# Kernel optimization log

Measured on AMD Instinct MI355X. Metric: run time of the kernel, lower is better.

Reference implementation:

```python
import jax, jax.numpy as jnp
import numpy as np

N, E = 50000, 800000
IN, HID, HEADS = 512, 64, 2
NEG_SLOPE = 0.2

def _p(key, shape, fan_in):
    return jax.random.normal(key, shape, dtype=jnp.float32) * (1.0 / np.sqrt(fan_in))

def setup_inputs() -> dict:
    key = jax.random.key(0)
    ks = jax.random.split(key, 16)
    x = jax.random.normal(ks[0], (N, IN), dtype=jnp.float32)
    edge_index = jax.random.randint(ks[1], (2, E), 0, N)
    d = dict(x=x, edge_index=edge_index)
    # layer 0: in -> hidden*heads
    d['W0'] = _p(ks[2], (IN, HEADS * HID), IN)
    d['a_src0'] = _p(ks[3], (HEADS, HID), HID)
    d['a_dst0'] = _p(ks[4], (HEADS, HID), HID)
    d['b0'] = jnp.zeros((HEADS * HID,), jnp.float32)
    # layer 1: hidden*heads -> hidden*heads
    d['W1'] = _p(ks[5], (HEADS * HID, HEADS * HID), HEADS * HID)
    d['a_src1'] = _p(ks[6], (HEADS, HID), HID)
    d['a_dst1'] = _p(ks[7], (HEADS, HID), HID)
    d['b1'] = jnp.zeros((HEADS * HID,), jnp.float32)
    # layer 2: hidden*heads -> hidden, heads=1
    d['W2'] = _p(ks[8], (HEADS * HID, HID), HEADS * HID)
    d['a_src2'] = _p(ks[9], (1, HID), HID)
    d['a_dst2'] = _p(ks[10], (1, HID), HID)
    d['b2'] = jnp.zeros((HID,), jnp.float32)
    # MLP heads
    d['Wv'] = _p(ks[11], (HID, HID), HID)
    d['bv'] = jnp.zeros((HID,), jnp.float32)
    d['Wt'] = _p(ks[12], (HID, HID), HID)
    d['bt'] = jnp.zeros((HID,), jnp.float32)
    return d

def gat_conv(x, src, dst, W, a_src, a_dst, b, n_nodes):
    # PyG GATConv: linear -> per-node att scores -> edge leaky_relu -> segment softmax over dst -> weighted scatter-sum
    H, C = a_src.shape
    h = (x @ W).reshape(n_nodes, H, C)                     # [N,H,C]
    s = jnp.einsum('nhc,hc->nh', h, a_src)                 # [N,H]
    t = jnp.einsum('nhc,hc->nh', h, a_dst)                 # [N,H]
    e = jax.nn.leaky_relu(s[src] + t[dst], NEG_SLOPE)      # [Etot,H]
    m = jax.ops.segment_max(e, dst, num_segments=n_nodes)  # stable softmax per dst
    ex = jnp.exp(e - m[dst])
    den = jax.ops.segment_sum(ex, dst, num_segments=n_nodes)
    alpha = ex / (den[dst] + 1e-16)                        # [Etot,H]
    out = jax.ops.segment_sum(h[src] * alpha[..., None], dst, num_segments=n_nodes)
    return out.reshape(n_nodes, H * C) + b

def reference(x, edge_index, W0, a_src0, a_dst0, b0, W1, a_src1, a_dst1, b1,
              W2, a_src2, a_dst2, b2, Wv, bv, Wt, bt):
    n = x.shape[0]
    loop = jnp.arange(n)
    src = jnp.concatenate([edge_index[0], loop])  # add_self_loops=True
    dst = jnp.concatenate([edge_index[1], loop])
    h = gat_conv(x, src, dst, W0, a_src0, a_dst0, b0, n)
    h = jax.nn.relu(h)
    h = gat_conv(h, src, dst, W1, a_src1, a_dst1, b1, n)
    h = jax.nn.relu(h)
    h = gat_conv(h, src, dst, W2, a_src2, a_dst2, b2, n)  # heads=1 -> [N,HID]
    x_vision = jax.nn.relu(h @ Wv + bv)
    x_text = jax.nn.relu(h @ Wt + bt)
    return (h, x_vision, x_text)
```

## Files before the change

kernel.cpp:

```cpp
#include <hip/hip_runtime.h>
#include <hip/hip_bf16.h>
#include <hip/hip_fp16.h>
#include <math.h>

#define NN 50000
#define NE 800000

typedef unsigned short ushort_t;
typedef unsigned int uint_t;
typedef __attribute__((ext_vector_type(8))) short bf16x8;
typedef __attribute__((ext_vector_type(4))) float f32x4;

__device__ __forceinline__ float lrelu(float x) { return x >= 0.f ? x : 0.2f * x; }

__device__ __forceinline__ ushort_t f2bf_rn(float f) {
  uint_t u = __builtin_bit_cast(uint_t, f);
  uint_t r = u + 0x7FFFu + ((u >> 16) & 1u);
  return (ushort_t)(r >> 16);
}
__device__ __forceinline__ float bf2f(ushort_t h) {
  uint_t u = ((uint_t)h) << 16;
  return __builtin_bit_cast(float, u);
}
__device__ __forceinline__ ushort_t f2h_bits(float f) {
  __half h = __float2half(f);
  return __builtin_bit_cast(ushort_t, h);
}

__global__ __launch_bounds__(256) void zero_kernel(int* __restrict__ p, int n) {
  int i = blockIdx.x * 256 + threadIdx.x;
  if (i < n) p[i] = 0;
}

__device__ __forceinline__ void prep_dev(const float* __restrict__ W, int Kdim, int C,
                                         ushort_t* __restrict__ wth, ushort_t* __restrict__ wtl,
                                         int t) {
  int nk = Kdim >> 4;
  if (t >= C * nk) return;
  int c = t / nk, kc = (t % nk) << 4;
  uint_t hw[8], lw[8];
#pragma unroll
  for (int i = 0; i < 8; ++i) {
    float f0 = W[(size_t)(kc + 2 * i) * C + c];
    float f1 = W[(size_t)(kc + 2 * i + 1) * C + c];
    ushort_t h0 = f2bf_rn(f0), h1 = f2bf_rn(f1);
    ushort_t l0 = f2bf_rn(f0 - bf2f(h0)), l1 = f2bf_rn(f1 - bf2f(h1));
    hw[i] = (uint_t)h0 | ((uint_t)h1 << 16);
    lw[i] = (uint_t)l0 | ((uint_t)l1 << 16);
  }
  uint_t* ph = (uint_t*)&wth[(size_t)c * Kdim + kc];
  uint_t* pl = (uint_t*)&wtl[(size_t)c * Kdim + kc];
  *(uint4*)ph = make_uint4(hw[0], hw[1], hw[2], hw[3]);
  *(uint4*)(ph + 4) = make_uint4(hw[4], hw[5], hw[6], hw[7]);
  *(uint4*)pl = make_uint4(lw[0], lw[1], lw[2], lw[3]);
  *(uint4*)(pl + 4) = make_uint4(lw[4], lw[5], lw[6], lw[7]);
}

#define CNT_BLOCKS 3125
__global__ __launch_bounds__(256) void setup_kernel(const int* __restrict__ ei,
                                                    int* __restrict__ counts,
                                                    const float* __restrict__ W0, ushort_t* wt0h, ushort_t* wt0l,
                                                    const float* __restrict__ W1, ushort_t* wt1h, ushort_t* wt1l,
                                                    const float* __restrict__ W2, ushort_t* wt2h, ushort_t* wt2l,
                                                    const float* __restrict__ Wv, const float* __restrict__ Wt,
                                                    ushort_t* wHh, ushort_t* wHl) {
  int b = blockIdx.x;
  if (b < CNT_BLOCKS) {
    int e = b * 256 + threadIdx.x;
    if (e < NE) atomicAdd(&counts[ei[NE + e]], 1);
    return;
  }
  b -= CNT_BLOCKS;
  if (b < 16) { prep_dev(W0, 512, 128, wt0h, wt0l, b * 256 + threadIdx.x); return; }
  b -= 16;
  if (b < 4) { prep_dev(W1, 128, 128, wt1h, wt1l, b * 256 + threadIdx.x); return; }
  b -= 4;
  if (b < 2) { prep_dev(W2, 128, 64, wt2h, wt2l, b * 256 + threadIdx.x); return; }
  b -= 2;
  if (b < 1) { prep_dev(Wv, 64, 64, wHh, wHl, b * 256 + threadIdx.x); return; }
  b -= 1;
  prep_dev(Wt, 64, 64, wHh + 64 * 64, wHl + 64 * 64, b * 256 + threadIdx.x);
}

__global__ __launch_bounds__(256) void scan_blocksum_kernel(const int* __restrict__ counts,
                                                            int* __restrict__ bsums, int n) {
  __shared__ int red[4];
  int i = blockIdx.x * 256 + threadIdx.x;
  int v = (i < n) ? counts[i] : 0;
#pragma unroll
  for (int off = 32; off > 0; off >>= 1) v += __shfl_down(v, off);
  if ((threadIdx.x & 63) == 0) red[threadIdx.x >> 6] = v;
  __syncthreads();
  if (threadIdx.x == 0) bsums[blockIdx.x] = red[0] + red[1] + red[2] + red[3];
}

__global__ __launch_bounds__(256) void scan_offsets_kernel(int* __restrict__ bsums, int nb) {
  __shared__ int sm[256];
  int tid = threadIdx.x;
  int v = (tid < nb) ? bsums[tid] : 0;
  sm[tid] = v;
  __syncthreads();
  for (int off = 1; off < 256; off <<= 1) {
    int u = (tid >= off) ? sm[tid - off] : 0;
    __syncthreads();
    sm[tid] += u;
    __syncthreads();
  }
  if (tid < nb) bsums[tid] = sm[tid] - v;
}

__global__ __launch_bounds__(256) void scan_final_kernel(const int* __restrict__ counts,
                                                         const int* __restrict__ boffs,
                                                         int* __restrict__ row_ptr,
                                                         int* __restrict__ cursor, int n, int E) {
  __shared__ int sm[256];
  int tid = threadIdx.x;
  int i = blockIdx.x * 256 + tid;
  int v = (i < n) ? counts[i] : 0;
  int orig = v;
  sm[tid] = v;
  __syncthreads();
  for (int off = 1; off < 256; off <<= 1) {
    int u = (tid >= off) ? sm[tid - off] : 0;
    __syncthreads();
    sm[tid] += u;
    __syncthreads();
  }
  if (i < n) {
    row_ptr[i] = boffs[blockIdx.x] + sm[tid] - orig;
    cursor[i] = 0;
  }
  if (i == n) row_ptr[n] = E;
}

__global__ void fill_kernel(const int* __restrict__ ei, const int* __restrict__ row_ptr,
                            int* __restrict__ cursor, int* __restrict__ col_src, int E) {
  int e = blockIdx.x * blockDim.x + threadIdx.x;
  if (e < E) {
    int d = ei[E + e];
    int pos = row_ptr[d] + atomicAdd(&cursor[d], 1);
    col_src[pos] = ei[e];
  }
}

template <int K, bool SPLIT>
__global__ __launch_bounds__(256, 4) void gemm_att128_kernel(const float* __restrict__ Af,
                                                             const ushort_t* __restrict__ Ahp,
                                                             const ushort_t* __restrict__ Alp,
                                                             const ushort_t* __restrict__ wth,
                                                             const ushort_t* __restrict__ wtl,
                                                             const float* __restrict__ a_src,
                                                             const float* __restrict__ a_dst,
                                                             __half2* __restrict__ h2h,
                                                             float* __restrict__ s_arr,
                                                             float* __restrict__ t_arr, int n) {
  __shared__ __align__(16) ushort_t smem[15360];
  ushort_t (*ah)[40] = (ushort_t(*)[40])smem;
  ushort_t (*al)[40] = (ushort_t(*)[40])(smem + 2560);
  ushort_t (*bh)[40] = (ushort_t(*)[40])(smem + 5120);
  ushort_t (*bl)[40] = (ushort_t(*)[40])(smem + 10240);

  const int t = threadIdx.x;
  const int row0 = blockIdx.x * 64;
  const int asrow = t >> 2, akc = (t & 3) * 8;
  const int bcol = t >> 1, bkc = (t & 1) * 16;

  const int lane = t & 63;
  const int wid = t >> 6;
  const int wm = wid >> 1, wn = wid & 1;
  const int r16 = lane & 15, g = lane >> 4;

  f32x4 acc[2][4];
#pragma unroll
  for (int i = 0; i < 2; ++i)
#pragma unroll
    for (int j = 0; j < 4; ++j) acc[i][j] = (f32x4)(0.f);

  for (int kt = 0; kt < K / 32; ++kt) {
    const int k0 = kt * 32;
    if (SPLIT) {
      uint4 vh = make_uint4(0, 0, 0, 0), vl = vh;
      if (row0 + asrow < n) {
        vh = *(const uint4*)&Ahp[(size_t)(row0 + asrow) * K + k0 + akc];
        vl = *(const uint4*)&Alp[(size_t)(row0 + asrow) * K + k0 + akc];
      }
      *(uint4*)&ah[asrow][akc] = vh;
      *(uint4*)&al[asrow][akc] = vl;
    } else {
      uint_t hw[4], lw[4];
      if (row0 + asrow < n) {
        const float* ap = &Af[(size_t)(row0 + asrow) * K + k0 + akc];
#pragma unroll
        for (int j = 0; j < 2; ++j) {
          float4 v = *(const float4*)(ap + j * 4);
          ushort_t h0 = f2bf_rn(v.x), h1 = f2bf_rn(v.y), h2 = f2bf_rn(v.z), h3 = f2bf_rn(v.w);
          ushort_t l0 = f2bf_rn(v.x - bf2f(h0)), l1 = f2bf_rn(v.y - bf2f(h1));
          ushort_t l2 = f2bf_rn(v.z - bf2f(h2)), l3 = f2bf_rn(v.w - bf2f(h3));
          hw[j * 2] = (uint_t)h0 | ((uint_t)h1 << 16);
          hw[j * 2 + 1] = (uint_t)h2 | ((uint_t)h3 << 16);
          lw[j * 2] = (uint_t)l0 | ((uint_t)l1 << 16);
          lw[j * 2 + 1] = (uint_t)l2 | ((uint_t)l3 << 16);
        }
      } else {
#pragma unroll
        for (int j = 0; j < 4; ++j) { hw[j] = 0; lw[j] = 0; }
      }
      *(uint4*)&ah[asrow][akc] = make_uint4(hw[0], hw[1], hw[2], hw[3]);
      *(uint4*)&al[asrow][akc] = make_uint4(lw[0], lw[1], lw[2], lw[3]);
    }
    {
      const ushort_t* ph = &wth[(size_t)bcol * K + k0 + bkc];
      const ushort_t* pl = &wtl[(size_t)bcol * K + k0 + bkc];
      *(uint4*)&bh[bcol][bkc] = *(const uint4*)ph;
      *(uint4*)&bh[bcol][bkc + 8] = *(const uint4*)(ph + 8);
      *(uint4*)&bl[bcol][bkc] = *(const uint4*)pl;
      *(uint4*)&bl[bcol][bkc + 8] = *(const uint4*)(pl + 8);
    }
    __syncthreads();

    bf16x8 fah[2], fal[2], fbh[4], fbl[4];
#pragma unroll
    for (int mf = 0; mf < 2; ++mf) {
      fah[mf] = *(const bf16x8*)&ah[wm * 32 + mf * 16 + r16][g * 8];
      fal[mf] = *(const bf16x8*)&al[wm * 32 + mf * 16 + r16][g * 8];
    }
#pragma unroll
    for (int nf = 0; nf < 4; ++nf) {
      fbh[nf] = *(const bf16x8*)&bh[wn * 64 + nf * 16 + r16][g * 8];
      fbl[nf] = *(const bf16x8*)&bl[wn * 64 + nf * 16 + r16][g * 8];
    }
#pragma unroll
    for (int mf = 0; mf < 2; ++mf)
#pragma unroll
      for (int nf = 0; nf < 4; ++nf) {
        acc[mf][nf] = __builtin_amdgcn_mfma_f32_16x16x32_bf16(fah[mf], fbh[nf], acc[mf][nf], 0, 0, 0);
        acc[mf][nf] = __builtin_amdgcn_mfma_f32_16x16x32_bf16(fah[mf], fbl[nf], acc[mf][nf], 0, 0, 0);
        acc[mf][nf] = __builtin_amdgcn_mfma_f32_16x16x32_bf16(fal[mf], fbh[nf], acc[mf][nf], 0, 0, 0);
      }
    __syncthreads();
  }

  const int head = wn;
  float asv[4], adv[4];
#pragma unroll
  for (int nf = 0; nf < 4; ++nf) {
    asv[nf] = a_src[head * 64 + nf * 16 + r16];
    adv[nf] = a_dst[head * 64 + nf * 16 + r16];
  }
#pragma unroll
  for (int mf = 0; mf < 2; ++mf) {
#pragma unroll
    for (int reg = 0; reg < 4; ++reg) {
      float sp = 0.f, tp = 0.f;
#pragma unroll
      for (int nf = 0; nf < 4; ++nf) {
        sp = fmaf(acc[mf][nf][reg], asv[nf], sp);
        tp = fmaf(acc[mf][nf][reg], adv[nf], tp);
      }
#pragma unroll
      for (int off = 1; off < 16; off <<= 1) {
        sp += __shfl_xor(sp, off);
        tp += __shfl_xor(tp, off);
      }
      int row = row0 + wm * 32 + mf * 16 + g * 4 + reg;
      if (r16 == 0 && row < n) {
        s_arr[row * 2 + head] = sp;
        t_arr[row * 2 + head] = tp;
      }
    }
  }

  ushort_t* hstage = smem;
#pragma unroll
  for (int mf = 0; mf < 2; ++mf)
#pragma unroll
    for (int nf = 0; nf < 4; ++nf)
#pragma unroll
      for (int reg = 0; reg < 4; ++reg) {
        int rl = wm * 32 + mf * 16 + g * 4 + reg;
        int col = (nf * 16 + r16) * 2 + head;
        hstage[rl * 136 + col] = f2h_bits(acc[mf][nf][reg]);
      }
  __syncthreads();
#pragma unroll
  for (int it = 0; it < 4; ++it) {
    int idx = t + it * 256;
    int r = idx >> 4, ch = idx & 15;
    if (row0 + r < n) {
      *(uint4*)((char*)h2h + (size_t)(row0 + r) * 256 + ch * 16) =
          *(const uint4*)&hstage[r * 136 + ch * 8];
    }
  }
}

__global__ __launch_bounds__(256, 4) void gemm_att64_kernel(const ushort_t* __restrict__ Ahp,
                                                            const ushort_t* __restrict__ Alp,
                                                            const ushort_t* __restrict__ wth,
                                                            const ushort_t* __restrict__ wtl,
                                                            const float* __restrict__ a_src,
                                                            const float* __restrict__ a_dst,
                                                            __half* __restrict__ h16,
                                                            float* __restrict__ s1,
                                                            float* __restrict__ t1, int n) {
  constexpr int K = 128;
  __shared__ __align__(16) ushort_t smem[10240];
  ushort_t (*ah)[40] = (ushort_t(*)[40])smem;
  ushort_t (*al)[40] = (ushort_t(*)[40])(smem + 2560);
  ushort_t (*bh)[40] = (ushort_t(*)[40])(smem + 5120);
  ushort_t (*bl)[40] = (ushort_t(*)[40])(smem + 7680);

  const int t = threadIdx.x;
  const int row0 = blockIdx.x * 64;
  const int asrow = t >> 2, akc = (t & 3) * 8;

  const int lane = t & 63;
  const int wid = t >> 6;
  const int r16 = lane & 15, g = lane >> 4;

  f32x4 acc[4];
#pragma unroll
  for (int j = 0; j < 4; ++j) acc[j] = (f32x4)(0.f);

  for (int kt = 0; kt < K / 32; ++kt) {
    const int k0 = kt * 32;
    {
      uint4 vh = make_uint4(0, 0, 0, 0), vl = vh;
      if (row0 + asrow < n) {
        vh = *(const uint4*)&Ahp[(size_t)(row0 + asrow) * K + k0 + akc];
        vl = *(const uint4*)&Alp[(size_t)(row0 + asrow) * K + k0 + akc];
      }
      *(uint4*)&ah[asrow][akc] = vh;
      *(uint4*)&al[asrow][akc] = vl;
    }
    {
      *(uint4*)&bh[asrow][akc] = *(const uint4*)&wth[(size_t)asrow * K + k0 + akc];
      *(uint4*)&bl[asrow][akc] = *(const uint4*)&wtl[(size_t)asrow * K + k0 + akc];
    }
    __syncthreads();

    bf16x8 fahv, falv, fbh[4], fbl[4];
    fahv = *(const bf16x8*)&ah[wid * 16 + r16][g * 8];
    falv = *(const bf16x8*)&al[wid * 16 + r16][g * 8];
#pragma unroll
    for (int nf = 0; nf < 4; ++nf) {
      fbh[nf] = *(const bf16x8*)&bh[nf * 16 + r16][g * 8];
      fbl[nf] = *(const bf16x8*)&bl[nf * 16 + r16][g * 8];
    }
#pragma unroll
    for (int nf = 0; nf < 4; ++nf) {
      acc[nf] = __builtin_amdgcn_mfma_f32_16x16x32_bf16(fahv, fbh[nf], acc[nf], 0, 0, 0);
      acc[nf] = __builtin_amdgcn_mfma_f32_16x16x32_bf16(fahv, fbl[nf], acc[nf], 0, 0, 0);
      acc[nf] = __builtin_amdgcn_mfma_f32_16x16x32_bf16(falv, fbh[nf], acc[nf], 0, 0, 0);
    }
    __syncthreads();
  }

  float asv[4], adv[4];
#pragma unroll
  for (int nf = 0; nf < 4; ++nf) {
    asv[nf] = a_src[nf * 16 + r16];
    adv[nf] = a_dst[nf * 16 + r16];
  }
#pragma unroll
  for (int reg = 0; reg < 4; ++reg) {
    float sp = 0.f, tp = 0.f;
#pragma unroll
    for (int nf = 0; nf < 4; ++nf) {
      sp = fmaf(acc[nf][reg], asv[nf], sp);
      tp = fmaf(acc[nf][reg], adv[nf], tp);
    }
#pragma unroll
    for (int off = 1; off < 16; off <<= 1) {
      sp += __shfl_xor(sp, off);
      tp += __shfl_xor(tp, off);
    }
    int row = row0 + wid * 16 + g * 4 + reg;
    if (r16 == 0 && row < n) {
      s1[row] = sp;
      t1[row] = tp;
    }
  }

  ushort_t* hstage = smem;
#pragma unroll
  for (int nf = 0; nf < 4; ++nf)
#pragma unroll
    for (int reg = 0; reg < 4; ++reg) {
      int rl = wid * 16 + g * 4 + reg;
      hstage[rl * 72 + nf * 16 + r16] = f2h_bits(acc[nf][reg]);
    }
  __syncthreads();
#pragma unroll
  for (int it = 0; it < 2; ++it) {
    int idx = t + it * 256;
    int r = idx >> 3, ch = idx & 7;
    if (row0 + r < n) {
      *(uint4*)((char*)h16 + (size_t)(row0 + r) * 128 + ch * 16) =
          *(const uint4*)&hstage[r * 72 + ch * 8];
    }
  }
}

__global__ __launch_bounds__(256, 4) void gemm_heads_kernel(const ushort_t* __restrict__ Ahp,
                                                            const ushort_t* __restrict__ Alp,
                                                            const ushort_t* __restrict__ wth,
                                                            const ushort_t* __restrict__ wtl,
                                                            const float* __restrict__ bv,
                                                            const float* __restrict__ bt,
                                                            float* __restrict__ out_v,
                                                            float* __restrict__ out_t, int n) {
  constexpr int K = 64;
  __shared__ __align__(16) ushort_t smem[15360];
  ushort_t (*ah)[40] = (ushort_t(*)[40])smem;
  ushort_t (*al)[40] = (ushort_t(*)[40])(smem + 2560);
  ushort_t (*bh)[40] = (ushort_t(*)[40])(smem + 5120);
  ushort_t (*bl)[40] = (ushort_t(*)[40])(smem + 10240);

  const int t = threadIdx.x;
  const int row0 = blockIdx.x * 64;
  const int asrow = t >> 2, akc = (t & 3) * 8;
  const int bcol = t >> 1, bkc = (t & 1) * 16;

  const int lane = t & 63;
  const int wid = t >> 6;
  const int wm = wid >> 1, wn = wid & 1;
  const int r16 = lane & 15, g = lane >> 4;

  f32x4 acc[2][4];
#pragma unroll
  for (int i = 0; i < 2; ++i)
#pragma unroll
    for (int j = 0; j < 4; ++j) acc[i][j] = (f32x4)(0.f);

  for (int kt = 0; kt < K / 32; ++kt) {
    const int k0 = kt * 32;
    {
      uint4 vh = make_uint4(0, 0, 0, 0), vl = vh;
      if (row0 + asrow < n) {
        vh = *(const uint4*)&Ahp[(size_t)(row0 + asrow) * K + k0 + akc];
        vl = *(const uint4*)&Alp[(size_t)(row0 + asrow) * K + k0 + akc];
      }
      *(uint4*)&ah[asrow][akc] = vh;
      *(uint4*)&al[asrow][akc] = vl;
    }
    {
      const ushort_t* ph = &wth[(size_t)bcol * K + k0 + bkc];
      const ushort_t* pl = &wtl[(size_t)bcol * K + k0 + bkc];
      *(uint4*)&bh[bcol][bkc] = *(const uint4*)ph;
      *(uint4*)&bh[bcol][bkc + 8] = *(const uint4*)(ph + 8);
      *(uint4*)&bl[bcol][bkc] = *(const uint4*)pl;
      *(uint4*)&bl[bcol][bkc + 8] = *(const uint4*)(pl + 8);
    }
    __syncthreads();

    bf16x8 fah[2], fal[2], fbh[4], fbl[4];
#pragma unroll
    for (int mf = 0; mf < 2; ++mf) {
      fah[mf] = *(const bf16x8*)&ah[wm * 32 + mf * 16 + r16][g * 8];
      fal[mf] = *(const bf16x8*)&al[wm * 32 + mf * 16 + r16][g * 8];
    }
#pragma unroll
    for (int nf = 0; nf < 4; ++nf) {
      fbh[nf] = *(const bf16x8*)&bh[wn * 64 + nf * 16 + r16][g * 8];
      fbl[nf] = *(const bf16x8*)&bl[wn * 64 + nf * 16 + r16][g * 8];
    }
#pragma unroll
    for (int mf = 0; mf < 2; ++mf)
#pragma unroll
      for (int nf = 0; nf < 4; ++nf) {
        acc[mf][nf] = __builtin_amdgcn_mfma_f32_16x16x32_bf16(fah[mf], fbh[nf], acc[mf][nf], 0, 0, 0);
        acc[mf][nf] = __builtin_amdgcn_mfma_f32_16x16x32_bf16(fah[mf], fbl[nf], acc[mf][nf], 0, 0, 0);
        acc[mf][nf] = __builtin_amdgcn_mfma_f32_16x16x32_bf16(fal[mf], fbh[nf], acc[mf][nf], 0, 0, 0);
      }
    __syncthreads();
  }

  const float* bias = wn ? bt : bv;
  float* outp = wn ? out_t : out_v;
#pragma unroll
  for (int mf = 0; mf < 2; ++mf) {
#pragma unroll
    for (int reg = 0; reg < 4; ++reg) {
      int row = row0 + wm * 32 + mf * 16 + g * 4 + reg;
      if (row < n) {
#pragma unroll
        for (int nf = 0; nf < 4; ++nf) {
          int c = nf * 16 + r16;
          outp[(size_t)row * 64 + c] = fmaxf(acc[mf][nf][reg] + bias[c], 0.f);
        }
      }
    }
  }
}

__global__ __launch_bounds__(256) void agg2_kernel(const __half2* __restrict__ h2h,
                                                   const float2* __restrict__ s2,
                                                   const float2* __restrict__ t2,
                                                   const int* __restrict__ row_ptr,
                                                   const int* __restrict__ col_src,
                                                   const float* __restrict__ bias,
                                                   ushort_t* __restrict__ outh,
                                                   ushort_t* __restrict__ outl, int n) {
  int wid = (blockIdx.x * 256 + threadIdx.x) >> 6;
  int lane = threadIdx.x & 63;
  if (wid >= n) return;
  const int node = wid;
  const float2 tt = t2[node];
  const float t0 = tt.x, t1 = tt.y;
  const int beg = row_ptr[node], end = row_ptr[node + 1];

  float2 sself = s2[node];
  const float e_self0 = lrelu(sself.x + t0);
  const float e_self1 = lrelu(sself.y + t1);

  const int i_own = beg + lane;
  int src_own = node;
  float e0_own = -1e30f, e1_own = -1e30f;
  if (i_own < end) {
    src_own = col_src[i_own];
    float2 sv = s2[src_own];
    e0_own = lrelu(sv.x + t0);
    e1_own = lrelu(sv.y + t1);
  }
  float m0 = fmaxf(e_self0, e0_own), m1 = fmaxf(e_self1, e1_own);
  for (int i = beg + 64 + lane; i < end; i += 64) {
    float2 sv = s2[col_src[i]];
    m0 = fmaxf(m0, lrelu(sv.x + t0));
    m1 = fmaxf(m1, lrelu(sv.y + t1));
  }
#pragma unroll
  for (int off = 32; off > 0; off >>= 1) {
    m0 = fmaxf(m0, __shfl_xor(m0, off));
    m1 = fmaxf(m1, __shfl_xor(m1, off));
  }

  float p0 = __expf(e_self0 - m0);
  float p1 = __expf(e_self1 - m1);
  float d0 = p0, d1 = p1;
  float2 hself = __half22float2(h2h[(size_t)node * 64 + lane]);
  float acc0 = p0 * hself.x;
  float acc1 = p1 * hself.y;

  for (int base = beg; base < end; base += 64) {
    int srcn;
    float q0, q1;
    if (base == beg) {
      srcn = src_own;
      q0 = (i_own < end) ? __expf(e0_own - m0) : 0.f;
      q1 = (i_own < end) ? __expf(e1_own - m1) : 0.f;
    } else {
      int i = base + lane;
      srcn = node;
      q0 = 0.f; q1 = 0.f;
      if (i < end) {
        srcn = col_src[i];
        float2 sv = s2[srcn];
        q0 = __expf(lrelu(sv.x + t0) - m0);
        q1 = __expf(lrelu(sv.y + t1) - m1);
      }
    }
    const int cnt = min(64, end - base);
    const int cnt4 = (cnt + 3) & ~3;
    int i0 = __shfl(srcn, 0), i1 = __shfl(srcn, 1), i2 = __shfl(srcn, 2), i3 = __shfl(srcn, 3);
    __half2 b0 = h2h[(size_t)i0 * 64 + lane];
    __half2 b1 = h2h[(size_t)i1 * 64 + lane];
    __half2 b2 = h2h[(size_t)i2 * 64 + lane];
    __half2 b3 = h2h[(size_t)i3 * 64 + lane];
    for (int j = 0; j < cnt4; j += 4) {
      float p00 = __shfl(q0, j),     p01 = __shfl(q1, j);
      float p10 = __shfl(q0, j + 1), p11 = __shfl(q1, j + 1);
      float p20 = __shfl(q0, j + 2), p21 = __shfl(q1, j + 2);
      float p30 = __shfl(q0, j + 3), p31 = __shfl(q1, j + 3);
      __half2 c0 = b0, c1 = b1, c2 = b2, c3 = b3;
      if (j + 4 < cnt4) {
        int n0 = __shfl(srcn, j + 4), n1 = __shfl(srcn, j + 5);
        int n2 = __shfl(srcn, j + 6), n3 = __shfl(srcn, j + 7);
        b0 = h2h[(size_t)n0 * 64 + lane];
        b1 = h2h[(size_t)n1 * 64 + lane];
        b2 = h2h[(size_t)n2 * 64 + lane];
        b3 = h2h[(size_t)n3 * 64 + lane];
      }
      float2 f0 = __half22float2(c0), f1 = __half22float2(c1);
      float2 f2 = __half22float2(c2), f3 = __half22float2(c3);
      d0 += p00 + p10 + p20 + p30;
      d1 += p01 + p11 + p21 + p31;
      acc0 = fmaf(p00, f0.x, acc0);
      acc1 = fmaf(p01, f0.y, acc1);
      acc0 = fmaf(p10, f1.x, acc0);
      acc1 = fmaf(p11, f1.y, acc1);
      acc0 = fmaf(p20, f2.x, acc0);
      acc1 = fmaf(p21, f2.y, acc1);
      acc0 = fmaf(p30, f3.x, acc0);
      acc1 = fmaf(p31, f3.y, acc1);
    }
  }

  float o0 = fmaxf(acc0 / (d0 + 1e-16f) + bias[lane], 0.f);
  float o1 = fmaxf(acc1 / (d1 + 1e-16f) + bias[64 + lane], 0.f);
  ushort_t h0h = f2bf_rn(o0), h1h = f2bf_rn(o1);
  outh[(size_t)node * 128 + lane] = h0h;
  outh[(size_t)node * 128 + 64 + lane] = h1h;
  outl[(size_t)node * 128 + lane] = f2bf_rn(o0 - bf2f(h0h));
  outl[(size_t)node * 128 + 64 + lane] = f2bf_rn(o1 - bf2f(h1h));
}

__global__ __launch_bounds__(256) void agg1_kernel(const __half* __restrict__ h16,
                                                   const float* __restrict__ s,
                                                   const float* __restrict__ t,
                                                   const int* __restrict__ row_ptr,
                                                   const int* __restrict__ col_src,
                                                   const float* __restrict__ bias,
                                                   float* __restrict__ out,
                                                   ushort_t* __restrict__ outh,
                                                   ushort_t* __restrict__ outl, int n) {
  int wid = (blockIdx.x * 256 + threadIdx.x) >> 6;
  int lane = threadIdx.x & 63;
  if (wid >= n) return;
  const int node = wid;
  const float t0 = t[node];
  const int beg = row_ptr[node], end = row_ptr[node + 1];

  const float e_self = lrelu(s[node] + t0);
  const int i_own = beg + lane;
  int src_own = node;
  float e_own = -1e30f;
  if (i_own < end) {
    src_own = col_src[i_own];
    e_own = lrelu(s[src_own] + t0);
  }
  float m0 = fmaxf(e_self, e_own);
  for (int i = beg + 64 + lane; i < end; i += 64) {
    m0 = fmaxf(m0, lrelu(s[col_src[i]] + t0));
  }
#pragma unroll
  for (int off = 32; off > 0; off >>= 1) m0 = fmaxf(m0, __shfl_xor(m0, off));

  float p = __expf(e_self - m0);
  float d0 = p;
  float acc0 = p * __half2float(h16[(size_t)node * 64 + lane]);

  for (int base = beg; base < end; base += 64) {
    int srcn;
    float q0;
    if (base == beg) {
      srcn = src_own;
      q0 = (i_own < end) ? __expf(e_own - m0) : 0.f;
    } else {
      int i = base + lane;
      srcn = node;
      q0 = 0.f;
      if (i < end) {
        srcn = col_src[i];
        q0 = __expf(lrelu(s[srcn] + t0) - m0);
      }
    }
    const int cnt = min(64, end - base);
    const int cnt4 = (cnt + 3) & ~3;
    int i0 = __shfl(srcn, 0), i1 = __shfl(srcn, 1), i2 = __shfl(srcn, 2), i3 = __shfl(srcn, 3);
    __half b0 = h16[(size_t)i0 * 64 + lane];
    __half b1 = h16[(size_t)i1 * 64 + lane];
    __half b2 = h16[(size_t)i2 * 64 + lane];
    __half b3 = h16[(size_t)i3 * 64 + lane];
    for (int j = 0; j < cnt4; j += 4) {
      float p0 = __shfl(q0, j),     p1 = __shfl(q0, j + 1);
      float p2 = __shfl(q0, j + 2), p3 = __shfl(q0, j + 3);
      float c0 = __half2float(b0), c1 = __half2float(b1);
      float c2 = __half2float(b2), c3 = __half2float(b3);
      if (j + 4 < cnt4) {
        int n0 = __shfl(srcn, j + 4), n1 = __shfl(srcn, j + 5);
        int n2 = __shfl(srcn, j + 6), n3 = __shfl(srcn, j + 7);
        b0 = h16[(size_t)n0 * 64 + lane];
        b1 = h16[(size_t)n1 * 64 + lane];
        b2 = h16[(size_t)n2 * 64 + lane];
        b3 = h16[(size_t)n3 * 64 + lane];
      }
      d0 += p0 + p1 + p2 + p3;
      acc0 = fmaf(p0, c0, acc0);
      acc0 = fmaf(p1, c1, acc0);
      acc0 = fmaf(p2, c2, acc0);
      acc0 = fmaf(p3, c3, acc0);
    }
  }
  float o = acc0 / (d0 + 1e-16f) + bias[lane];
  out[(size_t)node * 64 + lane] = o;
  ushort_t oh = f2bf_rn(o);
  outh[(size_t)node * 64 + lane] = oh;
  outl[(size_t)node * 64 + lane] = f2bf_rn(o - bf2f(oh));
}

extern "C" void kernel_launch(void* const* d_in, const int* in_sizes, int n_in,
                              void* d_out, int out_size, void* d_ws, size_t ws_size,
                              hipStream_t stream) {
  const float* x       = (const float*)d_in[0];
  const int*   ei      = (const int*)d_in[1];
  const float* W0      = (const float*)d_in[2];
  const float* a_src0  = (const float*)d_in[3];
  const float* a_dst0  = (const float*)d_in[4];
  const float* b0      = (const float*)d_in[5];
  const float* W1      = (const float*)d_in[6];
  const float* a_src1  = (const float*)d_in[7];
  const float* a_dst1  = (const float*)d_in[8];
  const float* b1      = (const float*)d_in[9];
  const float* W2      = (const float*)d_in[10];
  const float* a_src2  = (const float*)d_in[11];
  const float* a_dst2  = (const float*)d_in[12];
  const float* b2      = (const float*)d_in[13];
  const float* Wv      = (const float*)d_in[14];
  const float* bv      = (const float*)d_in[15];
  const float* Wt      = (const float*)d_in[16];
  const float* bt      = (const float*)d_in[17];

  const int n = NN, E = NE;
  const int NB = (n + 255) / 256;
  const int NBF = (n + 1 + 255) / 256;

  char* w = (char*)d_ws;
  int* counts  = (int*)w;   w += (size_t)n * 4;
  int* row_ptr = (int*)w;   w += (size_t)(n + 4) * 4;
  int* cursor  = (int*)w;   w += (size_t)n * 4;
  int* bsums   = (int*)w;   w += (size_t)256 * 4;
  int* col_src = (int*)w;   w += (size_t)E * 4;
  float* s_arr = (float*)w; w += (size_t)n * 2 * 4;
  float* t_arr = (float*)w; w += (size_t)n * 2 * 4;
  ushort_t* AhP = (ushort_t*)w; w += (size_t)n * 128 * 2;
  ushort_t* AlP = (ushort_t*)w; w += (size_t)n * 128 * 2;
  __half2* h2h = (__half2*)w; w += (size_t)n * 64 * 4;
  __half* h16  = (__half*)w; w += (size_t)n * 64 * 2;
  ushort_t* h64h = (ushort_t*)w; w += (size_t)n * 64 * 2;
  ushort_t* h64l = (ushort_t*)w; w += (size_t)n * 64 * 2;
  ushort_t* wt0h = (ushort_t*)w; w += (size_t)128 * 512 * 2;
  ushort_t* wt0l = (ushort_t*)w; w += (size_t)128 * 512 * 2;
  ushort_t* wt1h = (ushort_t*)w; w += (size_t)128 * 128 * 2;
  ushort_t* wt1l = (ushort_t*)w; w += (size_t)128 * 128 * 2;
  ushort_t* wt2h = (ushort_t*)w; w += (size_t)64 * 128 * 2;
  ushort_t* wt2l = (ushort_t*)w; w += (size_t)64 * 128 * 2;
  ushort_t* wHh  = (ushort_t*)w; w += (size_t)128 * 64 * 2;
  ushort_t* wHl  = (ushort_t*)w; w += (size_t)128 * 64 * 2;

  float* s1 = s_arr;
  float* t1 = t_arr;

  float* out_h = (float*)d_out;
  float* out_v = out_h + (size_t)n * 64;
  float* out_t = out_v + (size_t)n * 64;

  zero_kernel<<<NB, 256, 0, stream>>>(counts, n);
  setup_kernel<<<CNT_BLOCKS + 16 + 4 + 2 + 1 + 1, 256, 0, stream>>>(
      ei, counts, W0, wt0h, wt0l, W1, wt1h, wt1l, W2, wt2h, wt2l, Wv, Wt, wHh, wHl);
  scan_blocksum_kernel<<<NB, 256, 0, stream>>>(counts, bsums, n);
  scan_offsets_kernel<<<1, 256, 0, stream>>>(bsums, NB);
  scan_final_kernel<<<NBF, 256, 0, stream>>>(counts, bsums, row_ptr, cursor, n, E);
  fill_kernel<<<(E + 255) / 256, 256, 0, stream>>>(ei, row_ptr, cursor, col_src, E);

  const int wgrid = (n + 3) / 4;
  const int g64 = (n + 63) / 64;

  gemm_att128_kernel<512, false><<<g64, 256, 0, stream>>>(x, nullptr, nullptr, wt0h, wt0l,
                                                          a_src0, a_dst0, h2h, s_arr, t_arr, n);
  agg2_kernel<<<wgrid, 256, 0, stream>>>(h2h, (const float2*)s_arr, (const float2*)t_arr,
                                         row_ptr, col_src, b0, AhP, AlP, n);

  gemm_att128_kernel<128, true><<<g64, 256, 0, stream>>>(nullptr, AhP, AlP, wt1h, wt1l,
                                                         a_src1, a_dst1, h2h, s_arr, t_arr, n);
  agg2_kernel<<<wgrid, 256, 0, stream>>>(h2h, (const float2*)s_arr, (const float2*)t_arr,
                                         row_ptr, col_src, b1, AhP, AlP, n);

  gemm_att64_kernel<<<g64, 256, 0, stream>>>(AhP, AlP, wt2h, wt2l, a_src2, a_dst2,
                                             h16, s1, t1, n);
  agg1_kernel<<<wgrid, 256, 0, stream>>>(h16, s1, t1, row_ptr, col_src, b2,
                                         out_h, h64h, h64l, n);

  gemm_heads_kernel<<<g64, 256, 0, stream>>>(h64h, h64l, wHh, wHl, bv, bt, out_v, out_t, n);
}
```

Baseline: 300.6 us.

## Load GEMM MFMA fragments directly from global memory, dropping LDS staging

```diff
diff --git a/kernel.cpp b/kernel.cpp
--- a/kernel.cpp
+++ b/kernel.cpp
@@ -154,80 +154,68 @@
                                                              __half2* __restrict__ h2h,
                                                              float* __restrict__ s_arr,
                                                              float* __restrict__ t_arr, int n) {
-  __shared__ __align__(16) ushort_t smem[15360];
-  ushort_t (*ah)[40] = (ushort_t(*)[40])smem;
-  ushort_t (*al)[40] = (ushort_t(*)[40])(smem + 2560);
-  ushort_t (*bh)[40] = (ushort_t(*)[40])(smem + 5120);
-  ushort_t (*bl)[40] = (ushort_t(*)[40])(smem + 10240);
+  __shared__ __align__(16) ushort_t hstage[64 * 136];
 
   const int t = threadIdx.x;
   const int row0 = blockIdx.x * 64;
-  const int asrow = t >> 2, akc = (t & 3) * 8;
-  const int bcol = t >> 1, bkc = (t & 1) * 16;
-
   const int lane = t & 63;
   const int wid = t >> 6;
   const int wm = wid >> 1, wn = wid & 1;
   const int r16 = lane & 15, g = lane >> 4;
 
+  int arow[2];
+  bool aok[2];
+#pragma unroll
+  for (int mf = 0; mf < 2; ++mf) {
+    arow[mf] = row0 + wm * 32 + mf * 16 + r16;
+    aok[mf] = arow[mf] < n;
+  }
+
   f32x4 acc[2][4];
 #pragma unroll
   for (int i = 0; i < 2; ++i)
 #pragma unroll
     for (int j = 0; j < 4; ++j) acc[i][j] = (f32x4)(0.f);
 
+#pragma unroll 1
   for (int kt = 0; kt < K / 32; ++kt) {
     const int k0 = kt * 32;
-    if (SPLIT) {
-      uint4 vh = make_uint4(0, 0, 0, 0), vl = vh;
-      if (row0 + asrow < n) {
-        vh = *(const uint4*)&Ahp[(size_t)(row0 + asrow) * K + k0 + akc];
-        vl = *(const uint4*)&Alp[(size_t)(row0 + asrow) * K + k0 + akc];
-      }
-      *(uint4*)&ah[asrow][akc] = vh;
-      *(uint4*)&al[asrow][akc] = vl;
-    } else {
-      uint_t hw[4], lw[4];
-      if (row0 + asrow < n) {
-        const float* ap = &Af[(size_t)(row0 + asrow) * K + k0 + akc];
-#pragma unroll
-        for (int j = 0; j < 2; ++j) {
-          float4 v = *(const float4*)(ap + j * 4);
-          ushort_t h0 = f2bf_rn(v.x), h1 = f2bf_rn(v.y), h2 = f2bf_rn(v.z), h3 = f2bf_rn(v.w);
-          ushort_t l0 = f2bf_rn(v.x - bf2f(h0)), l1 = f2bf_rn(v.y - bf2f(h1));
-          ushort_t l2 = f2bf_rn(v.z - bf2f(h2)), l3 = f2bf_rn(v.w - bf2f(h3));
-          hw[j * 2] = (uint_t)h0 | ((uint_t)h1 << 16);
-          hw[j * 2 + 1] = (uint_t)h2 | ((uint_t)h3 << 16);
-          lw[j * 2] = (uint_t)l0 | ((uint_t)l1 << 16);
-          lw[j * 2 + 1] = (uint_t)l2 | ((uint_t)l3 << 16);
+    bf16x8 fah[2], fal[2], fbh[4], fbl[4];
+#pragma unroll
+    for (int nf = 0; nf < 4; ++nf) {
+      size_t off = (size_t)(wn * 64 + nf * 16 + r16) * K + k0 + g * 8;
+      fbh[nf] = *(const bf16x8*)&wth[off];
+      fbl[nf] = *(const bf16x8*)&wtl[off];
+    }
+#pragma unroll
+    for (int mf = 0; mf < 2; ++mf) {
+      if (SPLIT) {
+        if (aok[mf]) {
+          size_t off = (size_t)arow[mf] * K + k0 + g * 8;
+          fah[mf] = *(const bf16x8*)&Ahp[off];
+          fal[mf] = *(const bf16x8*)&Alp[off];
+        } else {
+          fah[mf] = (bf16x8)(short)0;
+          fal[mf] = (bf16x8)(short)0;
         }
       } else {
-#pragma unroll
-        for (int j = 0; j < 4; ++j) { hw[j] = 0; lw[j] = 0; }
-      }
-      *(uint4*)&ah[asrow][akc] = make_uint4(hw[0], hw[1], hw[2], hw[3]);
-      *(uint4*)&al[asrow][akc] = make_uint4(lw[0], lw[1], lw[2], lw[3]);
-    }
-    {
-      const ushort_t* ph = &wth[(size_t)bcol * K + k0 + bkc];
-      const ushort_t* pl = &wtl[(size_t)bcol * K + k0 + bkc];
-      *(uint4*)&bh[bcol][bkc] = *(const uint4*)ph;
-      *(uint4*)&bh[bcol][bkc + 8] = *(const uint4*)(ph + 8);
-      *(uint4*)&bl[bcol][bkc] = *(const uint4*)pl;
-      *(uint4*)&bl[bcol][bkc + 8] = *(const uint4*)(pl + 8);
-    }
-    __syncthreads();
-
-    bf16x8 fah[2], fal[2], fbh[4], fbl[4];
-#pragma unroll
-    for (int mf = 0; mf < 2; ++mf) {
-      fah[mf] = *(const bf16x8*)&ah[wm * 32 + mf * 16 + r16][g * 8];
-      fal[mf] = *(const bf16x8*)&al[wm * 32 + mf * 16 + r16][g * 8];
-    }
-#pragma unroll
-    for (int nf = 0; nf < 4; ++nf) {
-      fbh[nf] = *(const bf16x8*)&bh[wn * 64 + nf * 16 + r16][g * 8];
-      fbl[nf] = *(const bf16x8*)&bl[wn * 64 + nf * 16 + r16][g * 8];
+        float4 v0 = make_float4(0, 0, 0, 0), v1 = v0;
+        if (aok[mf]) {
+          const float* ap = &Af[(size_t)arow[mf] * K + k0 + g * 8];
+          v0 = *(const float4*)ap;
+          v1 = *(const float4*)(ap + 4);
+        }
+        float fv[8] = {v0.x, v0.y, v0.z, v0.w, v1.x, v1.y, v1.z, v1.w};
+        bf16x8 h, l;
+#pragma unroll
+        for (int j = 0; j < 8; ++j) {
+          ushort_t hb = f2bf_rn(fv[j]);
+          h[j] = (short)hb;
+          l[j] = (short)f2bf_rn(fv[j] - bf2f(hb));
+        }
+        fah[mf] = h;
+        fal[mf] = l;
+      }
     }
 #pragma unroll
     for (int mf = 0; mf < 2; ++mf)
@@ -237,7 +225,6 @@
         acc[mf][nf] = __builtin_amdgcn_mfma_f32_16x16x32_bf16(fah[mf], fbl[nf], acc[mf][nf], 0, 0, 0);
         acc[mf][nf] = __builtin_amdgcn_mfma_f32_16x16x32_bf16(fal[mf], fbh[nf], acc[mf][nf], 0, 0, 0);
       }
-    __syncthreads();
   }
 
   const int head = wn;
@@ -270,7 +257,6 @@
     }
   }
 
-  ushort_t* hstage = smem;
 #pragma unroll
   for (int mf = 0; mf < 2; ++mf)
 #pragma unroll
@@ -303,48 +289,38 @@
                                                             float* __restrict__ s1,
                                                             float* __restrict__ t1, int n) {
   constexpr int K = 128;
-  __shared__ __align__(16) ushort_t smem[10240];
-  ushort_t (*ah)[40] = (ushort_t(*)[40])smem;
-  ushort_t (*al)[40] = (ushort_t(*)[40])(smem + 2560);
-  ushort_t (*bh)[40] = (ushort_t(*)[40])(smem + 5120);
-  ushort_t (*bl)[40] = (ushort_t(*)[40])(smem + 7680);
+  __shared__ __align__(16) ushort_t hstage[64 * 72];
 
   const int t = threadIdx.x;
   const int row0 = blockIdx.x * 64;
-  const int asrow = t >> 2, akc = (t & 3) * 8;
-
   const int lane = t & 63;
   const int wid = t >> 6;
   const int r16 = lane & 15, g = lane >> 4;
 
+  const int arow = row0 + wid * 16 + r16;
+  const bool aok = arow < n;
+
   f32x4 acc[4];
 #pragma unroll
   for (int j = 0; j < 4; ++j) acc[j] = (f32x4)(0.f);
 
+#pragma unroll 1
   for (int kt = 0; kt < K / 32; ++kt) {
     const int k0 = kt * 32;
-    {
-      uint4 vh = make_uint4(0, 0, 0, 0), vl = vh;
-      if (row0 + asrow < n) {
-        vh = *(const uint4*)&Ahp[(size_t)(row0 + asrow) * K + k0 + akc];
-        vl = *(const uint4*)&Alp[(size_t)(row0 + asrow) * K + k0 + akc];
-      }
-      *(uint4*)&ah[asrow][akc] = vh;
-      *(uint4*)&al[asrow][akc] = vl;
-    }
-    {
-      *(uint4*)&bh[asrow][akc] = *(const uint4*)&wth[(size_t)asrow * K + k0 + akc];
-      *(uint4*)&bl[asrow][akc] = *(const uint4*)&wtl[(size_t)asrow * K + k0 + akc];
-    }
-    __syncthreads();
-
     bf16x8 fahv, falv, fbh[4], fbl[4];
-    fahv = *(const bf16x8*)&ah[wid * 16 + r16][g * 8];
-    falv = *(const bf16x8*)&al[wid * 16 + r16][g * 8];
+    if (aok) {
+      size_t off = (size_t)arow * K + k0 + g * 8;
+      fahv = *(const bf16x8*)&Ahp[off];
+      falv = *(const bf16x8*)&Alp[off];
+    } else {
+      fahv = (bf16x8)(short)0;
+      falv = (bf16x8)(short)0;
+    }
 #pragma unroll
     for (int nf = 0; nf < 4; ++nf) {
-      fbh[nf] = *(const bf16x8*)&bh[nf * 16 + r16][g * 8];
-      fbl[nf] = *(const bf16x8*)&bl[nf * 16 + r16][g * 8];
+      size_t off = (size_t)(nf * 16 + r16) * K + k0 + g * 8;
+      fbh[nf] = *(const bf16x8*)&wth[off];
+      fbl[nf] = *(const bf16x8*)&wtl[off];
     }
 #pragma unroll
     for (int nf = 0; nf < 4; ++nf) {
@@ -352,7 +328,6 @@
       acc[nf] = __builtin_amdgcn_mfma_f32_16x16x32_bf16(fahv, fbl[nf], acc[nf], 0, 0, 0);
       acc[nf] = __builtin_amdgcn_mfma_f32_16x16x32_bf16(falv, fbh[nf], acc[nf], 0, 0, 0);
     }
-    __syncthreads();
   }
 
   float asv[4], adv[4];
@@ -381,7 +356,6 @@
     }
   }
 
-  ushort_t* hstage = smem;
 #pragma unroll
   for (int nf = 0; nf < 4; ++nf)
 #pragma unroll
@@ -410,59 +384,47 @@
                                                             float* __restrict__ out_v,
                                                             float* __restrict__ out_t, int n) {
   constexpr int K = 64;
-  __shared__ __align__(16) ushort_t smem[15360];
-  ushort_t (*ah)[40] = (ushort_t(*)[40])smem;
-  ushort_t (*al)[40] = (ushort_t(*)[40])(smem + 2560);
-  ushort_t (*bh)[40] = (ushort_t(*)[40])(smem + 5120);
-  ushort_t (*bl)[40] = (ushort_t(*)[40])(smem + 10240);
-
   const int t = threadIdx.x;
   const int row0 = blockIdx.x * 64;
-  const int asrow = t >> 2, akc = (t & 3) * 8;
-  const int bcol = t >> 1, bkc = (t & 1) * 16;
-
   const int lane = t & 63;
   const int wid = t >> 6;
   const int wm = wid >> 1, wn = wid & 1;
   const int r16 = lane & 15, g = lane >> 4;
 
+  int arow[2];
+  bool aok[2];
+#pragma unroll
+  for (int mf = 0; mf < 2; ++mf) {
+    arow[mf] = row0 + wm * 32 + mf * 16 + r16;
+    aok[mf] = arow[mf] < n;
+  }
+
   f32x4 acc[2][4];
 #pragma unroll
   for (int i = 0; i < 2; ++i)
 #pragma unroll
     for (int j = 0; j < 4; ++j) acc[i][j] = (f32x4)(0.f);
 
+#pragma unroll 1
   for (int kt = 0; kt < K / 32; ++kt) {
     const int k0 = kt * 32;
-    {
-      uint4 vh = make_uint4(0, 0, 0, 0), vl = vh;
-      if (row0 + asrow < n) {
-        vh = *(const uint4*)&Ahp[(size_t)(row0 + asrow) * K + k0 + akc];
-        vl = *(const uint4*)&Alp[(size_t)(row0 + asrow) * K + k0 + akc];
-      }
-      *(uint4*)&ah[asrow][akc] = vh;
-      *(uint4*)&al[asrow][akc] = vl;
-    }
-    {
-      const ushort_t* ph = &wth[(size_t)bcol * K + k0 + bkc];
-      const ushort_t* pl = &wtl[(size_t)bcol * K + k0 + bkc];
-      *(uint4*)&bh[bcol][bkc] = *(const uint4*)ph;
-      *(uint4*)&bh[bcol][bkc + 8] = *(const uint4*)(ph + 8);
-      *(uint4*)&bl[bcol][bkc] = *(const uint4*)pl;
-      *(uint4*)&bl[bcol][bkc + 8] = *(const uint4*)(pl + 8);
-    }
-    __syncthreads();
-
     bf16x8 fah[2], fal[2], fbh[4], fbl[4];
 #pragma unroll
+    for (int nf = 0; nf < 4; ++nf) {
+      size_t off = (size_t)(wn * 64 + nf * 16 + r16) * K + k0 + g * 8;
+      fbh[nf] = *(const bf16x8*)&wth[off];
+      fbl[nf] = *(const bf16x8*)&wtl[off];
+    }
+#pragma unroll
     for (int mf = 0; mf < 2; ++mf) {
-      fah[mf] = *(const bf16x8*)&ah[wm * 32 + mf * 16 + r16][g * 8];
-      fal[mf] = *(const bf16x8*)&al[wm * 32 + mf * 16 + r16][g * 8];
-    }
-#pragma unroll
-    for (int nf = 0; nf < 4; ++nf) {
-      fbh[nf] = *(const bf16x8*)&bh[wn * 64 + nf * 16 + r16][g * 8];
-      fbl[nf] = *(const bf16x8*)&bl[wn * 64 + nf * 16 + r16][g * 8];
+      if (aok[mf]) {
+        size_t off = (size_t)arow[mf] * K + k0 + g * 8;
+        fah[mf] = *(const bf16x8*)&Ahp[off];
+        fal[mf] = *(const bf16x8*)&Alp[off];
+      } else {
+        fah[mf] = (bf16x8)(short)0;
+        fal[mf] = (bf16x8)(short)0;
+      }
     }
 #pragma unroll
     for (int mf = 0; mf < 2; ++mf)
@@ -472,7 +434,6 @@
         acc[mf][nf] = __builtin_amdgcn_mfma_f32_16x16x32_bf16(fah[mf], fbl[nf], acc[mf][nf], 0, 0, 0);
         acc[mf][nf] = __builtin_amdgcn_mfma_f32_16x16x32_bf16(fal[mf], fbh[nf], acc[mf][nf], 0, 0, 0);
       }
-    __syncthreads();
   }
 
   const float* bias = wn ? bt : bv;
```

Result: slower. 379.3 us (+26.2%).

## Replace per-node softmax max pass with global source-score upper bound

Applied to the files above, without the earlier changes.

```diff
diff --git a/kernel.cpp b/kernel.cpp
--- a/kernel.cpp
+++ b/kernel.cpp
@@ -26,10 +26,20 @@
   __half h = __float2half(f);
   return __builtin_bit_cast(ushort_t, h);
 }
-
-__global__ __launch_bounds__(256) void zero_kernel(int* __restrict__ p, int n) {
+__device__ __forceinline__ uint_t fkey(float f) {
+  uint_t b = __builtin_bit_cast(uint_t, f);
+  return (b & 0x80000000u) ? ~b : (b | 0x80000000u);
+}
+__device__ __forceinline__ float fdec(uint_t k) {
+  uint_t b = (k & 0x80000000u) ? (k & 0x7fffffffu) : ~k;
+  return __builtin_bit_cast(float, b);
+}
+
+__global__ __launch_bounds__(256) void zero_kernel(int* __restrict__ p, int n,
+                                                   uint_t* __restrict__ keys) {
   int i = blockIdx.x * 256 + threadIdx.x;
   if (i < n) p[i] = 0;
+  if (blockIdx.x == 0 && threadIdx.x < 8) keys[threadIdx.x] = 0;
 }
 
 __device__ __forceinline__ void prep_dev(const float* __restrict__ W, int Kdim, int C,
@@ -153,7 +163,8 @@
                                                              const float* __restrict__ a_dst,
                                                              __half2* __restrict__ h2h,
                                                              float* __restrict__ s_arr,
-                                                             float* __restrict__ t_arr, int n) {
+                                                             float* __restrict__ t_arr,
+                                                             uint_t* __restrict__ smax, int n) {
   __shared__ __align__(16) ushort_t smem[15360];
   ushort_t (*ah)[40] = (ushort_t(*)[40])smem;
   ushort_t (*al)[40] = (ushort_t(*)[40])(smem + 2560);
@@ -247,6 +258,7 @@
     asv[nf] = a_src[head * 64 + nf * 16 + r16];
     adv[nf] = a_dst[head * 64 + nf * 16 + r16];
   }
+  float smax_local = -3.4e38f;
 #pragma unroll
   for (int mf = 0; mf < 2; ++mf) {
 #pragma unroll
@@ -262,6 +274,7 @@
         sp += __shfl_xor(sp, off);
         tp += __shfl_xor(tp, off);
       }
+      smax_local = fmaxf(smax_local, sp);
       int row = row0 + wm * 32 + mf * 16 + g * 4 + reg;
       if (r16 == 0 && row < n) {
         s_arr[row * 2 + head] = sp;
@@ -269,6 +282,9 @@
       }
     }
   }
+  smax_local = fmaxf(smax_local, __shfl_xor(smax_local, 16));
+  smax_local = fmaxf(smax_local, __shfl_xor(smax_local, 32));
+  if (lane == 0) atomicMax(&smax[head], fkey(smax_local));
 
   ushort_t* hstage = smem;
 #pragma unroll
@@ -301,7 +317,8 @@
                                                             const float* __restrict__ a_dst,
                                                             __half* __restrict__ h16,
                                                             float* __restrict__ s1,
-                                                            float* __restrict__ t1, int n) {
+                                                            float* __restrict__ t1,
+                                                            uint_t* __restrict__ smax, int n) {
   constexpr int K = 128;
   __shared__ __align__(16) ushort_t smem[10240];
   ushort_t (*ah)[40] = (ushort_t(*)[40])smem;
@@ -312,6 +329,7 @@
   const int t = threadIdx.x;
   const int row0 = blockIdx.x * 64;
   const int asrow = t >> 2, akc = (t & 3) * 8;
+  const bool arow_ok = (row0 + asrow) < n;
 
   const int lane = t & 63;
   const int wid = t >> 6;
@@ -325,7 +343,7 @@
     const int k0 = kt * 32;
     {
       uint4 vh = make_uint4(0, 0, 0, 0), vl = vh;
-      if (row0 + asrow < n) {
+      if (arow_ok) {
         vh = *(const uint4*)&Ahp[(size_t)(row0 + asrow) * K + k0 + akc];
         vl = *(const uint4*)&Alp[(size_t)(row0 + asrow) * K + k0 + akc];
       }
@@ -361,6 +379,7 @@
     asv[nf] = a_src[nf * 16 + r16];
     adv[nf] = a_dst[nf * 16 + r16];
   }
+  float smax_local = -3.4e38f;
 #pragma unroll
   for (int reg = 0; reg < 4; ++reg) {
     float sp = 0.f, tp = 0.f;
@@ -374,12 +393,16 @@
       sp += __shfl_xor(sp, off);
       tp += __shfl_xor(tp, off);
     }
+    smax_local = fmaxf(smax_local, sp);
     int row = row0 + wid * 16 + g * 4 + reg;
     if (r16 == 0 && row < n) {
       s1[row] = sp;
       t1[row] = tp;
     }
   }
+  smax_local = fmaxf(smax_local, __shfl_xor(smax_local, 16));
+  smax_local = fmaxf(smax_local, __shfl_xor(smax_local, 32));
+  if (lane == 0) atomicMax(smax, fkey(smax_local));
 
   ushort_t* hstage = smem;
 #pragma unroll
@@ -420,6 +443,7 @@
   const int row0 = blockIdx.x * 64;
   const int asrow = t >> 2, akc = (t & 3) * 8;
   const int bcol = t >> 1, bkc = (t & 1) * 16;
+  const bool arow_ok = (row0 + asrow) < n;
 
   const int lane = t & 63;
   const int wid = t >> 6;
@@ -436,7 +460,7 @@
     const int k0 = kt * 32;
     {
       uint4 vh = make_uint4(0, 0, 0, 0), vl = vh;
-      if (row0 + asrow < n) {
+      if (arow_ok) {
         vh = *(const uint4*)&Ahp[(size_t)(row0 + asrow) * K + k0 + akc];
         vl = *(const uint4*)&Alp[(size_t)(row0 + asrow) * K + k0 + akc];
       }
@@ -499,65 +523,40 @@
                                                    const int* __restrict__ row_ptr,
                                                    const int* __restrict__ col_src,
                                                    const float* __restrict__ bias,
+                                                   const uint_t* __restrict__ smax,
                                                    ushort_t* __restrict__ outh,
                                                    ushort_t* __restrict__ outl, int n) {
   int wid = (blockIdx.x * 256 + threadIdx.x) >> 6;
   int lane = threadIdx.x & 63;
   if (wid >= n) return;
   const int node = wid;
+  const float smax0 = fdec(smax[0]);
+  const float smax1 = fdec(smax[1]);
   const float2 tt = t2[node];
   const float t0 = tt.x, t1 = tt.y;
+  const float m0 = lrelu(smax0 + t0);
+  const float m1 = lrelu(smax1 + t1);
   const int beg = row_ptr[node], end = row_ptr[node + 1];
 
   float2 sself = s2[node];
-  const float e_self0 = lrelu(sself.x + t0);
-  const float e_self1 = lrelu(sself.y + t1);
-
-  const int i_own = beg + lane;
-  int src_own = node;
-  float e0_own = -1e30f, e1_own = -1e30f;
-  if (i_own < end) {
-    src_own = col_src[i_own];
-    float2 sv = s2[src_own];
-    e0_own = lrelu(sv.x + t0);
-    e1_own = lrelu(sv.y + t1);
-  }
-  float m0 = fmaxf(e_self0, e0_own), m1 = fmaxf(e_self1, e1_own);
-  for (int i = beg + 64 + lane; i < end; i += 64) {
-    float2 sv = s2[col_src[i]];
-    m0 = fmaxf(m0, lrelu(sv.x + t0));
-    m1 = fmaxf(m1, lrelu(sv.y + t1));
-  }
-#pragma unroll
-  for (int off = 32; off > 0; off >>= 1) {
-    m0 = fmaxf(m0, __shfl_xor(m0, off));
-    m1 = fmaxf(m1, __shfl_xor(m1, off));
-  }
-
-  float p0 = __expf(e_self0 - m0);
-  float p1 = __expf(e_self1 - m1);
-  float d0 = p0, d1 = p1;
+  float p0 = __expf(lrelu(sself.x + t0) - m0);
+  float p1 = __expf(lrelu(sself.y + t1) - m1);
+  float dp0 = 0.f, dp1 = 0.f;
   float2 hself = __half22float2(h2h[(size_t)node * 64 + lane]);
   float acc0 = p0 * hself.x;
   float acc1 = p1 * hself.y;
 
   for (int base = beg; base < end; base += 64) {
-    int srcn;
-    float q0, q1;
-    if (base == beg) {
-      srcn = src_own;
-      q0 = (i_own < end) ? __expf(e0_own - m0) : 0.f;
-      q1 = (i_own < end) ? __expf(e1_own - m1) : 0.f;
-    } else {
-      int i = base + lane;
-      srcn = node;
-      q0 = 0.f; q1 = 0.f;
-      if (i < end) {
-        srcn = col_src[i];
-        float2 sv = s2[srcn];
-        q0 = __expf(lrelu(sv.x + t0) - m0);
-        q1 = __expf(lrelu(sv.y + t1) - m1);
-      }
+    int i = base + lane;
+    int srcn = node;
+    float q0 = 0.f, q1 = 0.f;
+    if (i < end) {
+      srcn = col_src[i];
+      float2 sv = s2[srcn];
+      q0 = __expf(lrelu(sv.x + t0) - m0);
+      q1 = __expf(lrelu(sv.y + t1) - m1);
+      dp0 += q0;
+      dp1 += q1;
     }
     const int cnt = min(64, end - base);
     const int cnt4 = (cnt + 3) & ~3;
@@ -582,8 +581,6 @@
       }
       float2 f0 = __half22float2(c0), f1 = __half22float2(c1);
       float2 f2 = __half22float2(c2), f3 = __half22float2(c3);
-      d0 += p00 + p10 + p20 + p30;
-      d1 += p01 + p11 + p21 + p31;
       acc0 = fmaf(p00, f0.x, acc0);
       acc1 = fmaf(p01, f0.y, acc1);
       acc0 = fmaf(p10, f1.x, acc0);
@@ -595,6 +592,14 @@
     }
   }
 
+#pragma unroll
+  for (int off = 32; off > 0; off >>= 1) {
+    dp0 += __shfl_xor(dp0, off);
+    dp1 += __shfl_xor(dp1, off);
+  }
+  const float d0 = dp0 + p0;
+  const float d1 = dp1 + p1;
+
   float o0 = fmaxf(acc0 / (d0 + 1e-16f) + bias[lane], 0.f);
   float o1 = fmaxf(acc1 / (d1 + 1e-16f) + bias[64 + lane], 0.f);
   ushort_t h0h = f2bf_rn(o0), h1h = f2bf_rn(o1);
@@ -610,6 +615,7 @@
                                                    const int* __restrict__ row_ptr,
                                                    const int* __restrict__ col_src,
                                                    const float* __restrict__ bias,
+                                                   const uint_t* __restrict__ smax,
                                                    float* __restrict__ out,
                                                    ushort_t* __restrict__ outh,
                                                    ushort_t* __restrict__ outl, int n) {
@@ -618,41 +624,21 @@
   if (wid >= n) return;
   const int node = wid;
   const float t0 = t[node];
+  const float m0 = lrelu(fdec(smax[0]) + t0);
   const int beg = row_ptr[node], end = row_ptr[node + 1];
 
-  const float e_self = lrelu(s[node] + t0);
-  const int i_own = beg + lane;
-  int src_own = node;
-  float e_own = -1e30f;
-  if (i_own < end) {
-    src_own = col_src[i_own];
-    e_own = lrelu(s[src_own] + t0);
-  }
-  float m0 = fmaxf(e_self, e_own);
-  for (int i = beg + 64 + lane; i < end; i += 64) {
-    m0 = fmaxf(m0, lrelu(s[col_src[i]] + t0));
-  }
-#pragma unroll
-  for (int off = 32; off > 0; off >>= 1) m0 = fmaxf(m0, __shfl_xor(m0, off));
-
-  float p = __expf(e_self - m0);
-  float d0 = p;
+  float p = __expf(lrelu(s[node] + t0) - m0);
+  float dp = 0.f;
   float acc0 = p * __half2float(h16[(size_t)node * 64 + lane]);
 
   for (int base = beg; base < end; base += 64) {
-    int srcn;
-    float q0;
-    if (base == beg) {
-      srcn = src_own;
-      q0 = (i_own < end) ? __expf(e_own - m0) : 0.f;
-    } else {
-      int i = base + lane;
-      srcn = node;
-      q0 = 0.f;
-      if (i < end) {
-        srcn = col_src[i];
-        q0 = __expf(lrelu(s[srcn] + t0) - m0);
-      }
+    int i = base + lane;
+    int srcn = node;
+    float q0 = 0.f;
+    if (i < end) {
+      srcn = col_src[i];
+      q0 = __expf(lrelu(s[srcn] + t0) - m0);
+      dp += q0;
     }
     const int cnt = min(64, end - base);
     const int cnt4 = (cnt + 3) & ~3;
@@ -674,13 +660,16 @@
         b2 = h16[(size_t)n2 * 64 + lane];
         b3 = h16[(size_t)n3 * 64 + lane];
       }
-      d0 += p0 + p1 + p2 + p3;
       acc0 = fmaf(p0, c0, acc0);
       acc0 = fmaf(p1, c1, acc0);
       acc0 = fmaf(p2, c2, acc0);
       acc0 = fmaf(p3, c3, acc0);
     }
   }
+#pragma unroll
+  for (int off = 32; off > 0; off >>= 1) dp += __shfl_xor(dp, off);
+  const float d0 = dp + p;
+
   float o = acc0 / (d0 + 1e-16f) + bias[lane];
   out[(size_t)node * 64 + lane] = o;
   ushort_t oh = f2bf_rn(o);
@@ -719,6 +708,7 @@
   int* row_ptr = (int*)w;   w += (size_t)(n + 4) * 4;
   int* cursor  = (int*)w;   w += (size_t)n * 4;
   int* bsums   = (int*)w;   w += (size_t)256 * 4;
+  uint_t* smax = (uint_t*)w; w += (size_t)8 * 4;
   int* col_src = (int*)w;   w += (size_t)E * 4;
   float* s_arr = (float*)w; w += (size_t)n * 2 * 4;
   float* t_arr = (float*)w; w += (size_t)n * 2 * 4;
@@ -744,7 +734,7 @@
   float* out_v = out_h + (size_t)n * 64;
   float* out_t = out_v + (size_t)n * 64;
 
-  zero_kernel<<<NB, 256, 0, stream>>>(counts, n);
+  zero_kernel<<<NB, 256, 0, stream>>>(counts, n, smax);
   setup_kernel<<<CNT_BLOCKS + 16 + 4 + 2 + 1 + 1, 256, 0, stream>>>(
       ei, counts, W0, wt0h, wt0l, W1, wt1h, wt1l, W2, wt2h, wt2l, Wv, Wt, wHh, wHl);
   scan_blocksum_kernel<<<NB, 256, 0, stream>>>(counts, bsums, n);
@@ -756,18 +746,20 @@
   const int g64 = (n + 63) / 64;
 
   gemm_att128_kernel<512, false><<<g64, 256, 0, stream>>>(x, nullptr, nullptr, wt0h, wt0l,
-                                                          a_src0, a_dst0, h2h, s_arr, t_arr, n);
+                                                          a_src0, a_dst0, h2h, s_arr, t_arr,
+                                                          smax + 0, n);
   agg2_kernel<<<wgrid, 256, 0, stream>>>(h2h, (const float2*)s_arr, (const float2*)t_arr,
-                                         row_ptr, col_src, b0, AhP, AlP, n);
+                                         row_ptr, col_src, b0, smax + 0, AhP, AlP, n);
 
   gemm_att128_kernel<128, true><<<g64, 256, 0, stream>>>(nullptr, AhP, AlP, wt1h, wt1l,
-                                                         a_src1, a_dst1, h2h, s_arr, t_arr, n);
+                                                         a_src1, a_dst1, h2h, s_arr, t_arr,
+                                                         smax + 2, n);
   agg2_kernel<<<wgrid, 256, 0, stream>>>(h2h, (const float2*)s_arr, (const float2*)t_arr,
-                                         row_ptr, col_src, b1, AhP, AlP, n);
+                                         row_ptr, col_src, b1, smax + 2, AhP, AlP, n);
 
   gemm_att64_kernel<<<g64, 256, 0, stream>>>(AhP, AlP, wt2h, wt2l, a_src2, a_dst2,
-                                             h16, s1, t1, n);
-  agg1_kernel<<<wgrid, 256, 0, stream>>>(h16, s1, t1, row_ptr, col_src, b2,
+                                             h16, s1, t1, smax + 4, n);
+  agg1_kernel<<<wgrid, 256, 0, stream>>>(h16, s1, t1, row_ptr, col_src, b2, smax + 4,
                                          out_h, h64h, h64l, n);
 
   gemm_heads_kernel<<<g64, 256, 0, stream>>>(h64h, h64l, wHh, wHl, bv, bt, out_v, out_t, n);
```

After: 391.4 us. 1.3x slower.
